# Performance work log

Hardware: AMD Instinct MI355X
Metric: run time of the kernel (lower is better)

## Reference

```python
import jax, jax.numpy as jnp
import numpy as np

B, NU, NT = 128, 32, 64          # batch, users/sample, antennas/sample
IN_F, H, OUT_F, NL = 128, 128, 16, 2
N_U, N_A = B * NU, B * NT        # total user / antenna nodes


def setup_inputs() -> dict:
    key = jax.random.key(0)
    ks = iter(jax.random.split(key, 40))
    p = lambda shape: jax.random.normal(next(ks), shape, jnp.float32) * 0.05
    inp = {
        'user_feat': jax.random.normal(next(ks), (N_U, IN_F), jnp.float32),
        'ant_noise': jax.random.normal(next(ks), (N_A, H), jnp.float32),
    }
    # complete bipartite edges within each batch sample
    b = np.arange(B)[:, None, None]
    u = np.arange(NU)[None, :, None]
    t = np.arange(NT)[None, None, :]
    su = np.broadcast_to(b * NU + u, (B, NU, NT)).reshape(-1)  # user global ids
    dt = np.broadcast_to(b * NT + t, (B, NU, NT)).reshape(-1)  # antenna global ids
    inp['src_u2a'] = jnp.asarray(su, jnp.int32)
    inp['dst_u2a'] = jnp.asarray(dt, jnp.int32)
    inp['src_a2u'] = jnp.asarray(dt, jnp.int32)
    inp['dst_a2u'] = jnp.asarray(su, jnp.int32)
    inp['W_ue'] = p((IN_F, H)); inp['b_ue'] = p((H,))
    inp['W_t'] = p((H, H));     inp['b_t'] = p((H,))
    for name in ['ca_aggr', 'ca_self', 'ca_comb', 'cu_aggr', 'cu_self', 'cu_comb']:
        inp[name + '_W'] = p((NL, H, H))
        inp[name + '_b'] = p((NL, H))
    inp['W_norm'] = p((H, OUT_F)); inp['b_norm'] = p((OUT_F,))
    return inp


def mlp(x, W, b):
    # stack of NL Linear(H,H) + ReLU, as in MLP module
    for i in range(W.shape[0]):
        x = jax.nn.relu(x @ W[i] + b[i])
    return x


def rel_conv(src_f, dst_f, src_idx, dst_idx, n_dst, aW, ab, sW, sb, cW, cb):
    # GraphConv2: mean-aggregate mlp_aggr(src) over in-edges, combine with mlp_self(dst)
    msg = mlp(src_f, aW, ab)                                   # [n_src, H]
    summed = jax.ops.segment_sum(msg[src_idx], dst_idx, num_segments=n_dst)
    deg = jax.ops.segment_sum(jnp.ones(dst_idx.shape, jnp.float32), dst_idx,
                              num_segments=n_dst)
    mean = summed / jnp.maximum(deg, 1.0)[:, None]
    return mlp(mlp(dst_f, sW, sb) + mean, cW, cb)


def reference(user_feat, ant_noise, src_u2a, dst_u2a, src_a2u, dst_a2u,
              W_ue, b_ue, W_t, b_t,
              ca_aggr_W, ca_aggr_b, ca_self_W, ca_self_b, ca_comb_W, ca_comb_b,
              cu_aggr_W, cu_aggr_b, cu_self_W, cu_self_b, cu_comb_W, cu_comb_b,
              W_norm, b_norm):
    # InitLayer
    hu = jax.nn.relu(user_feat @ W_ue + b_ue)                  # [B*NU, H]
    ant = jax.nn.relu(hu.reshape(B, NU, H).mean(axis=1) @ W_t + b_t)  # [B, H]
    ha = jnp.repeat(ant, NT, axis=0) + ant_noise               # [B*NT, H]
    # two applications of the SAME HeteroGraphConv (shared weights)
    for _ in range(2):
        na = rel_conv(hu, ha, src_u2a, dst_u2a, N_A,
                      ca_aggr_W, ca_aggr_b, ca_self_W, ca_self_b, ca_comb_W, ca_comb_b)
        nu = rel_conv(ha, hu, src_a2u, dst_a2u, N_U,
                      cu_aggr_W, cu_aggr_b, cu_self_W, cu_self_b, cu_comb_W, cu_comb_b)
        hu, ha = nu, na
    # NormLayer: project, split real/imag, normalize to unit modulus
    y = (ha @ W_norm + b_norm).reshape(B, NT, OUT_F)
    rf = OUT_F // 2
    re, im = y[..., :rf], y[..., rf:]
    mag = jnp.sqrt(re * re + im * im)
    return jnp.concatenate([re / mag, im / mag], axis=-1)      # [B, NT, OUT_F]
```

## Files before the change

kernel.cpp:

```cpp
#include <hip/hip_runtime.h>
#include <math.h>


using frag  = __attribute__((ext_vector_type(8))) short;
using f32x4 = __attribute__((ext_vector_type(4))) float;

#define LDST 136
#define SCOPE_AGT __HIP_MEMORY_SCOPE_AGENT

__device__ __forceinline__ float  bf2f(ushort u) { return __uint_as_float(((unsigned)u) << 16); }
__device__ __forceinline__ ushort f2bf(float f) {
    unsigned u = __float_as_uint(f);
    u += 0x7fff + ((u >> 16) & 1);
    return (ushort)(u >> 16);
}
__device__ __forceinline__ void gst4_sc(void* p, unsigned v) {
    asm volatile("global_store_dword %0, %1, off sc1" :: "v"(p), "v"(v) : "memory");
}

struct GP {
    const float *uf, *noise, *b_ue, *W_t, *b_t;
    const float *bias6[6];
    const float *Wn, *bn;
    const ushort *Wp;
    float *out;
    float *pE, *pA0, *pU0, *pA1;
    unsigned *flg;
};

struct PrepP { const float* Wm[13]; ushort* Wp; };

__global__ __launch_bounds__(512) void k_prep(PrepP Q)
{
    const int t  = blockIdx.x * 512 + threadIdx.x;
    const int j  = t & 7, l = (t >> 3) & 63, w = (t >> 9) & 7,
              kc = (t >> 12) & 3, m = t >> 14;
    const float v = Q.Wm[m][(kc * 32 + (l >> 4) * 8 + j) * 128 + w * 16 + (l & 15)];
    Q.Wp[t] = f2bf(v);
}

__device__ __forceinline__ void psync(unsigned* myf, unsigned* pf, unsigned s) {
    asm volatile("s_waitcnt vmcnt(0)" ::: "memory");
    __syncthreads();
    if (threadIdx.x == 0) {
        __hip_atomic_store(myf, s, __ATOMIC_RELAXED, SCOPE_AGT);
        while (__hip_atomic_load(pf, __ATOMIC_RELAXED, SCOPE_AGT) < s)
            __builtin_amdgcn_s_sleep(1);
    }
    __syncthreads();
}

struct AF { frag f[4]; };
__device__ __forceinline__ AF ldA(const ushort* __restrict__ Wp, int mat, int tid)
{
    AF a;
    const ushort* base = Wp + ((size_t)mat << 14) + (tid << 3);
#pragma unroll
    for (int kc = 0; kc < 4; ++kc)
        a.f[kc] = *(const frag*)(base + (kc << 12));
    return a;
}

template<int MT, bool MEANADD>
__device__ __forceinline__ void mlp_stage(const AF& A, const ushort* Xl, ushort* Yl,
    const float* biasL, const float* meanL, int n0, int l15, int q)
{
    const float4 bv = *(const float4*)(biasL + n0 + q * 4);
    float4 mv = {0.f, 0.f, 0.f, 0.f};
    if (MEANADD) mv = *(const float4*)(meanL + n0 + q * 4);
#pragma unroll
    for (int mt = 0; mt < MT; ++mt) {
        frag Bv[4];
#pragma unroll
        for (int kc = 0; kc < 4; ++kc)
            Bv[kc] = *(const frag*)(Xl + (mt * 16 + l15) * LDST + kc * 32 + q * 8);
        f32x4 acc = {0.f, 0.f, 0.f, 0.f};
#pragma unroll
        for (int kc = 0; kc < 4; ++kc)
            acc = __builtin_amdgcn_mfma_f32_16x16x32_bf16(A.f[kc], Bv[kc], acc, 0, 0, 0);
        float v0 = acc[0] + bv.x, v1 = acc[1] + bv.y, v2 = acc[2] + bv.z, v3 = acc[3] + bv.w;
        v0 = v0 > 0.f ? v0 : 0.f; v1 = v1 > 0.f ? v1 : 0.f;
        v2 = v2 > 0.f ? v2 : 0.f; v3 = v3 > 0.f ? v3 : 0.f;
        if (MEANADD) { v0 += mv.x; v1 += mv.y; v2 += mv.z; v3 += mv.w; }
        ushort4 o = { f2bf(v0), f2bf(v1), f2bf(v2), f2bf(v3) };
        *(ushort4*)(Yl + (mt * 16 + l15) * LDST + n0 + q * 4) = o;
    }
}

template<int ROWS>
__device__ __forceinline__ void colsum(const ushort* buf, float* redL,
                                       float* ownDst, float* __restrict__ gDst)
{
    const int t = threadIdx.x, g = t >> 7, col = t & 127;
    float s = 0.f;
#pragma unroll
    for (int r = g; r < ROWS; r += 4) s += bf2f(buf[r * LDST + col]);
    redL[g * 128 + col] = s;
    __syncthreads();
    if (t < 128) {
        float tot = redL[t] + redL[128 + t] + redL[256 + t] + redL[384 + t];
        ownDst[t] = tot;
        gst4_sc(gDst + t, __float_as_uint(tot));
    }
    __syncthreads();
}

__global__ __launch_bounds__(512, 1) void k_gnn(GP P)
{
    __shared__ __align__(16) ushort HU[16 * LDST];
    __shared__ __align__(16) ushort HA[32 * LDST];
    __shared__ __align__(16) ushort T0[32 * LDST];
    __shared__ __align__(16) ushort T1[32 * LDST];
    __shared__ __align__(16) float  biasL[1792];
    __shared__ __align__(16) float  redL[512];
    __shared__ __align__(16) float  meanP[128], meanQ[128], antL[128];

    const int blk = blockIdx.x, tid = threadIdx.x;
    const int b = blk & 127, half = blk >> 7, prt = blk ^ 128;
    const int lane = tid & 63, wave = tid >> 6;
    const int q = lane >> 4, l15 = lane & 15;
    const int n0 = wave * 16;
    unsigned* myf = P.flg + blk * 32;
    unsigned* prf = P.flg + prt * 32;

    AF An = ldA(P.Wp, 12, tid);

    {
        const int r = tid >> 5, k4 = tid & 31;
        const float4 v = *(const float4*)(P.uf + (size_t)(b * 32 + half * 16 + r) * 128 + k4 * 4);
        ushort4 o = { f2bf(v.x), f2bf(v.y), f2bf(v.z), f2bf(v.w) };
        *(ushort4*)(T0 + r * LDST + k4 * 4) = o;
    }
#pragma unroll
    for (int c = tid; c < 1024; c += 512) {
        const int r = c >> 5, k4 = c & 31;
        const float4 v = *(const float4*)(P.noise + (size_t)(b * 64 + half * 32 + r) * 128 + k4 * 4);
        ushort4 o = { f2bf(v.x), f2bf(v.y), f2bf(v.z), f2bf(v.w) };
        *(ushort4*)(HA + r * LDST + k4 * 4) = o;
    }
    if (tid < 128) biasL[tid] = P.b_ue[tid];
    if (tid < 128) biasL[1664 + tid] = P.b_t[tid];
#pragma unroll
    for (int r = 0; r < 6; ++r)
        if (tid < 256) biasL[128 + r * 256 + tid] = P.bias6[r][tid];
    __syncthreads();

    AF A;
    A = An; An = ldA(P.Wp, 0, tid);
    mlp_stage<1, false>(A, T0, HU, biasL + 0, nullptr, n0, l15, q);
    __syncthreads();
    colsum<16>(HU, redL, meanP, P.pE + blk * 128);
    A = An; An = ldA(P.Wp, 1, tid);
    mlp_stage<1, false>(A, HU, T0, biasL + 128, nullptr, n0, l15, q);
    __syncthreads();
    A = An; An = ldA(P.Wp, 6, tid);
    mlp_stage<1, false>(A, T0, T1, biasL + 256, nullptr, n0, l15, q);
    __syncthreads();
    colsum<16>(T1, redL, meanQ, P.pA0 + blk * 128);
    psync(myf, prf, 1u);

    if (tid < 128) {
        meanP[tid] = (meanP[tid] + P.pE[prt * 128 + tid]) * (1.f / 32.f);
        meanQ[tid] = (meanQ[tid] + P.pA0[prt * 128 + tid]) * (1.f / 32.f);
    }
    __syncthreads();
    {
        const int g = tid >> 7, col = tid & 127;
        float s = 0.f;
#pragma unroll 4
        for (int k = g * 32; k < g * 32 + 32; ++k) s += meanP[k] * P.W_t[k * 128 + col];
        redL[g * 128 + col] = s;
    }
    __syncthreads();
    if (tid < 128) {
        float a = biasL[1664 + tid] + redL[tid] + redL[128 + tid] + redL[256 + tid] + redL[384 + tid];
        antL[tid] = a > 0.f ? a : 0.f;
    }
    __syncthreads();
#pragma unroll
    for (int c = tid; c < 1024; c += 512) {
        const int r = c >> 5, k4 = c & 31;
        ushort4 h = *(ushort4*)(HA + r * LDST + k4 * 4);
        ushort4 o = { f2bf(bf2f(h.x) + antL[k4 * 4 + 0]), f2bf(bf2f(h.y) + antL[k4 * 4 + 1]),
                      f2bf(bf2f(h.z) + antL[k4 * 4 + 2]), f2bf(bf2f(h.w) + antL[k4 * 4 + 3]) };
        *(ushort4*)(HA + r * LDST + k4 * 4) = o;
    }
    __syncthreads();

    A = An; An = ldA(P.Wp, 7, tid);
    mlp_stage<2, false>(A, HA, T0, biasL + 896, nullptr, n0, l15, q);
    __syncthreads();
    A = An; An = ldA(P.Wp, 2, tid);
    mlp_stage<2, false>(A, T0, T1, biasL + 1024, nullptr, n0, l15, q);
    __syncthreads();
    colsum<32>(T1, redL, meanP, P.pU0 + blk * 128);
    A = An; An = ldA(P.Wp, 3, tid);
    mlp_stage<2, false>(A, HA, T0, biasL + 384, nullptr, n0, l15, q);
    __syncthreads();
    psync(myf, prf, 2u);
    if (tid < 128)
        meanP[tid] = (meanP[tid] + P.pU0[prt * 128 + tid]) * (1.f / 64.f);
    __syncthreads();
    A = An; An = ldA(P.Wp, 4, tid);
    mlp_stage<2, true >(A, T0, T1, biasL + 512, meanQ, n0, l15, q);
    __syncthreads();
    A = An; An = ldA(P.Wp, 5, tid);
    mlp_stage<2, false>(A, T1, T0, biasL + 640, nullptr, n0, l15, q);
    __syncthreads();
    A = An; An = ldA(P.Wp, 8, tid);
    mlp_stage<2, false>(A, T0, HA, biasL + 768, nullptr, n0, l15, q);
    __syncthreads();
    A = An; An = ldA(P.Wp, 9, tid);
    mlp_stage<1, false>(A, HU, T0, biasL + 1152, nullptr, n0, l15, q);
    __syncthreads();
    A = An; An = ldA(P.Wp, 10, tid);
    mlp_stage<1, true >(A, T0, T1, biasL + 1280, meanP, n0, l15, q);
    __syncthreads();
    A = An; An = ldA(P.Wp, 11, tid);
    mlp_stage<1, false>(A, T1, T0, biasL + 1408, nullptr, n0, l15, q);
    __syncthreads();
    A = An; An = ldA(P.Wp, 0, tid);
    mlp_stage<1, false>(A, T0, HU, biasL + 1536, nullptr, n0, l15, q);
    __syncthreads();

    A = An; An = ldA(P.Wp, 1, tid);
    mlp_stage<1, false>(A, HU, T0, biasL + 128, nullptr, n0, l15, q);
    __syncthreads();
    A = An; An = ldA(P.Wp, 2, tid);
    mlp_stage<1, false>(A, T0, T1, biasL + 256, nullptr, n0, l15, q);
    __syncthreads();
    colsum<16>(T1, redL, meanQ, P.pA1 + blk * 128);
    A = An; An = ldA(P.Wp, 3, tid);
    mlp_stage<2, false>(A, HA, T0, biasL + 384, nullptr, n0, l15, q);
    __syncthreads();
    psync(myf, prf, 3u);
    if (tid < 128)
        meanQ[tid] = (meanQ[tid] + P.pA1[prt * 128 + tid]) * (1.f / 32.f);
    __syncthreads();
    A = An; An = ldA(P.Wp, 4, tid);
    mlp_stage<2, true >(A, T0, T1, biasL + 512, meanQ, n0, l15, q);
    __syncthreads();
    A = An; An = ldA(P.Wp, 5, tid);
    mlp_stage<2, false>(A, T1, T0, biasL + 640, nullptr, n0, l15, q);
    __syncthreads();
    A = An;
    mlp_stage<2, false>(A, T0, T1, biasL + 768, nullptr, n0, l15, q);
    __syncthreads();

    float* WnS = (float*)T0;
    *(float4*)(WnS + tid * 4) = *(const float4*)(P.Wn + tid * 4);
    __syncthreads();
    {
        const int row = tid >> 4, j = tid & 15;
        float acc = P.bn[j];
        const ushort* h = T1 + row * LDST;
#pragma unroll 8
        for (int k = 0; k < 128; ++k) acc += bf2f(h[k]) * WnS[k * 16 + j];
        const float other = __shfl_xor(acc, 8);
        const float mag = sqrtf(acc * acc + other * other);
        P.out[(size_t)(b * 64 + half * 32 + row) * 16 + j] = acc / mag;
    }
}

extern "C" void kernel_launch(void* const* d_in, const int* in_sizes, int n_in,
                              void* d_out, int out_size, void* d_ws, size_t ws_size,
                              hipStream_t stream)
{
    GP P;
    P.uf    = (const float*)d_in[0];
    P.noise = (const float*)d_in[1];
    const float* W_ue = (const float*)d_in[6];
    P.b_ue  = (const float*)d_in[7];
    P.W_t   = (const float*)d_in[8];
    P.b_t   = (const float*)d_in[9];
    const float* caW[3] = {(const float*)d_in[10], (const float*)d_in[12], (const float*)d_in[14]};
    const float* cab[3] = {(const float*)d_in[11], (const float*)d_in[13], (const float*)d_in[15]};
    const float* cuW[3] = {(const float*)d_in[16], (const float*)d_in[18], (const float*)d_in[20]};
    const float* cub[3] = {(const float*)d_in[17], (const float*)d_in[19], (const float*)d_in[21]};
    P.Wn  = (const float*)d_in[22];
    P.bn  = (const float*)d_in[23];
    P.out = (float*)d_out;

    PrepP Q;
    Q.Wm[0]  = caW[0]; Q.Wm[1]  = caW[0] + 16384;
    Q.Wm[2]  = caW[1]; Q.Wm[3]  = caW[1] + 16384;
    Q.Wm[4]  = caW[2]; Q.Wm[5]  = caW[2] + 16384;
    Q.Wm[6]  = cuW[0]; Q.Wm[7]  = cuW[0] + 16384;
    Q.Wm[8]  = cuW[1]; Q.Wm[9]  = cuW[1] + 16384;
    Q.Wm[10] = cuW[2]; Q.Wm[11] = cuW[2] + 16384;
    Q.Wm[12] = W_ue;
    P.bias6[0] = cab[0]; P.bias6[1] = cab[1]; P.bias6[2] = cab[2];
    P.bias6[3] = cub[0]; P.bias6[4] = cub[1]; P.bias6[5] = cub[2];

    char* w = (char*)d_ws;
    P.flg = (unsigned*)w;
    P.pE  = (float*)(w + 32768);
    P.pA0 = P.pE  + 256 * 128;
    P.pU0 = P.pA0 + 256 * 128;
    P.pA1 = P.pU0 + 256 * 128;
    ushort* Wp = (ushort*)(w + 32768 + 4 * 256 * 128 * 4);
    Q.Wp = Wp;
    P.Wp = Wp;

    k_prep<<<dim3(416), dim3(512), 0, stream>>>(Q);
    hipMemsetAsync(w, 0, 32768, stream);
    k_gnn<<<dim3(256), dim3(512), 0, stream>>>(P);
}
```

Baseline: 124.8 us.

## Fuse column sums into MLP epilogue, pack bf16 conversions, fold flag reset into prep

Column sums are now computed from fp32 accumulators inside the MLP stage epilogue with wave shuffles, so the separate LDS column-sum pass and its two barriers go away. Float-to-bf16 conversion uses the hardware packed v_cvt_pk_bf16_f32 instruction instead of manual rounding. The weight prep kernel now handles eight elements per thread with 16-byte stores (fewer blocks) and also zeroes the sync flags, which removes the separate memset launch. Column sums are now taken before bf16 rounding, so the means differ slightly from the old ones.

```diff
diff --git a/kernel.cpp b/kernel.cpp
--- a/kernel.cpp
+++ b/kernel.cpp
@@ -14,8 +14,13 @@
     u += 0x7fff + ((u >> 16) & 1);
     return (ushort)(u >> 16);
 }
-__device__ __forceinline__ void gst4_sc(void* p, unsigned v) {
-    asm volatile("global_store_dword %0, %1, off sc1" :: "v"(p), "v"(v) : "memory");
+__device__ __forceinline__ unsigned cvtpk(float lo, float hi) {
+    unsigned r;
+    asm("v_cvt_pk_bf16_f32 %0, %1, %2" : "=v"(r) : "v"(lo), "v"(hi));
+    return r;
+}
+__device__ __forceinline__ void gst16_sc(void* p, f32x4 v) {
+    asm volatile("global_store_dwordx4 %0, %1, off sc1" :: "v"(p), "v"(v) : "memory");
 }
 
 struct GP {
@@ -28,15 +33,21 @@
     unsigned *flg;
 };
 
-struct PrepP { const float* Wm[13]; ushort* Wp; };
+struct PrepP { const float* Wm[13]; ushort* Wp; unsigned* flg; };
 
 __global__ __launch_bounds__(512) void k_prep(PrepP Q)
 {
-    const int t  = blockIdx.x * 512 + threadIdx.x;
-    const int j  = t & 7, l = (t >> 3) & 63, w = (t >> 9) & 7,
-              kc = (t >> 12) & 3, m = t >> 14;
-    const float v = Q.Wm[m][(kc * 32 + (l >> 4) * 8 + j) * 128 + w * 16 + (l & 15)];
-    Q.Wp[t] = f2bf(v);
+    const int tid = threadIdx.x, blk = blockIdx.x;
+    if (blk < 16) Q.flg[blk * 512 + tid] = 0;
+    const int e = (blk * 512 + tid) * 8;
+    const int l = (e >> 3) & 63, w = (e >> 9) & 7, kc = (e >> 12) & 3, m = e >> 14;
+    const float* src = Q.Wm[m] + (kc * 32 + (l >> 4) * 8) * 128 + w * 16 + (l & 15);
+    ushort h[8];
+#pragma unroll
+    for (int j = 0; j < 8; ++j) h[j] = f2bf(src[j * 128]);
+    uint4 o = { (unsigned)h[0] | ((unsigned)h[1] << 16), (unsigned)h[2] | ((unsigned)h[3] << 16),
+                (unsigned)h[4] | ((unsigned)h[5] << 16), (unsigned)h[6] | ((unsigned)h[7] << 16) };
+    *(uint4*)(Q.Wp + e) = o;
 }
 
 __device__ __forceinline__ void psync(unsigned* myf, unsigned* pf, unsigned s) {
@@ -61,13 +72,15 @@
     return a;
 }
 
-template<int MT, bool MEANADD>
+template<int MT, bool MEANADD, bool CS>
 __device__ __forceinline__ void mlp_stage(const AF& A, const ushort* Xl, ushort* Yl,
-    const float* biasL, const float* meanL, int n0, int l15, int q)
+    const float* biasL, const float* meanL, float* csL, float* __restrict__ csG,
+    int n0, int l15, int q)
 {
     const float4 bv = *(const float4*)(biasL + n0 + q * 4);
     float4 mv = {0.f, 0.f, 0.f, 0.f};
     if (MEANADD) mv = *(const float4*)(meanL + n0 + q * 4);
+    float cs0 = 0.f, cs1 = 0.f, cs2 = 0.f, cs3 = 0.f;
 #pragma unroll
     for (int mt = 0; mt < MT; ++mt) {
         frag Bv[4];
@@ -82,27 +95,22 @@
         v0 = v0 > 0.f ? v0 : 0.f; v1 = v1 > 0.f ? v1 : 0.f;
         v2 = v2 > 0.f ? v2 : 0.f; v3 = v3 > 0.f ? v3 : 0.f;
         if (MEANADD) { v0 += mv.x; v1 += mv.y; v2 += mv.z; v3 += mv.w; }
-        ushort4 o = { f2bf(v0), f2bf(v1), f2bf(v2), f2bf(v3) };
-        *(ushort4*)(Yl + (mt * 16 + l15) * LDST + n0 + q * 4) = o;
-    }
-}
-
-template<int ROWS>
-__device__ __forceinline__ void colsum(const ushort* buf, float* redL,
-                                       float* ownDst, float* __restrict__ gDst)
-{
-    const int t = threadIdx.x, g = t >> 7, col = t & 127;
-    float s = 0.f;
-#pragma unroll
-    for (int r = g; r < ROWS; r += 4) s += bf2f(buf[r * LDST + col]);
-    redL[g * 128 + col] = s;
-    __syncthreads();
-    if (t < 128) {
-        float tot = redL[t] + redL[128 + t] + redL[256 + t] + redL[384 + t];
-        ownDst[t] = tot;
-        gst4_sc(gDst + t, __float_as_uint(tot));
-    }
-    __syncthreads();
+        if (CS) { cs0 += v0; cs1 += v1; cs2 += v2; cs3 += v3; }
+        uint2 o = { cvtpk(v0, v1), cvtpk(v2, v3) };
+        *(uint2*)(Yl + (mt * 16 + l15) * LDST + n0 + q * 4) = o;
+    }
+    if (CS) {
+#pragma unroll
+        for (int m = 1; m <= 8; m <<= 1) {
+            cs0 += __shfl_xor(cs0, m); cs1 += __shfl_xor(cs1, m);
+            cs2 += __shfl_xor(cs2, m); cs3 += __shfl_xor(cs3, m);
+        }
+        if (l15 == 0) {
+            f32x4 t = { cs0, cs1, cs2, cs3 };
+            *(f32x4*)(csL + n0 + q * 4) = t;
+            gst16_sc(csG + n0 + q * 4, t);
+        }
+    }
 }
 
 __global__ __launch_bounds__(512, 1) void k_gnn(GP P)
@@ -128,15 +136,15 @@
     {
         const int r = tid >> 5, k4 = tid & 31;
         const float4 v = *(const float4*)(P.uf + (size_t)(b * 32 + half * 16 + r) * 128 + k4 * 4);
-        ushort4 o = { f2bf(v.x), f2bf(v.y), f2bf(v.z), f2bf(v.w) };
-        *(ushort4*)(T0 + r * LDST + k4 * 4) = o;
+        uint2 o = { cvtpk(v.x, v.y), cvtpk(v.z, v.w) };
+        *(uint2*)(T0 + r * LDST + k4 * 4) = o;
     }
 #pragma unroll
     for (int c = tid; c < 1024; c += 512) {
         const int r = c >> 5, k4 = c & 31;
         const float4 v = *(const float4*)(P.noise + (size_t)(b * 64 + half * 32 + r) * 128 + k4 * 4);
-        ushort4 o = { f2bf(v.x), f2bf(v.y), f2bf(v.z), f2bf(v.w) };
-        *(ushort4*)(HA + r * LDST + k4 * 4) = o;
+        uint2 o = { cvtpk(v.x, v.y), cvtpk(v.z, v.w) };
+        *(uint2*)(HA + r * LDST + k4 * 4) = o;
     }
     if (tid < 128) biasL[tid] = P.b_ue[tid];
     if (tid < 128) biasL[1664 + tid] = P.b_t[tid];
@@ -147,16 +155,14 @@
 
     AF A;
     A = An; An = ldA(P.Wp, 0, tid);
-    mlp_stage<1, false>(A, T0, HU, biasL + 0, nullptr, n0, l15, q);
-    __syncthreads();
-    colsum<16>(HU, redL, meanP, P.pE + blk * 128);
+    mlp_stage<1, false, true>(A, T0, HU, biasL + 0, nullptr, meanP, P.pE + blk * 128, n0, l15, q);
+    __syncthreads();
     A = An; An = ldA(P.Wp, 1, tid);
-    mlp_stage<1, false>(A, HU, T0, biasL + 128, nullptr, n0, l15, q);
+    mlp_stage<1, false, false>(A, HU, T0, biasL + 128, nullptr, nullptr, nullptr, n0, l15, q);
     __syncthreads();
     A = An; An = ldA(P.Wp, 6, tid);
-    mlp_stage<1, false>(A, T0, T1, biasL + 256, nullptr, n0, l15, q);
-    __syncthreads();
-    colsum<16>(T1, redL, meanQ, P.pA0 + blk * 128);
+    mlp_stage<1, false, true>(A, T0, T1, biasL + 256, nullptr, meanQ, P.pA0 + blk * 128, n0, l15, q);
+    __syncthreads();
     psync(myf, prf, 1u);
 
     if (tid < 128) {
@@ -181,70 +187,68 @@
     for (int c = tid; c < 1024; c += 512) {
         const int r = c >> 5, k4 = c & 31;
         ushort4 h = *(ushort4*)(HA + r * LDST + k4 * 4);
-        ushort4 o = { f2bf(bf2f(h.x) + antL[k4 * 4 + 0]), f2bf(bf2f(h.y) + antL[k4 * 4 + 1]),
-                      f2bf(bf2f(h.z) + antL[k4 * 4 + 2]), f2bf(bf2f(h.w) + antL[k4 * 4 + 3]) };
-        *(ushort4*)(HA + r * LDST + k4 * 4) = o;
+        uint2 o = { cvtpk(bf2f(h.x) + antL[k4 * 4 + 0], bf2f(h.y) + antL[k4 * 4 + 1]),
+                    cvtpk(bf2f(h.z) + antL[k4 * 4 + 2], bf2f(h.w) + antL[k4 * 4 + 3]) };
+        *(uint2*)(HA + r * LDST + k4 * 4) = o;
     }
     __syncthreads();
 
     A = An; An = ldA(P.Wp, 7, tid);
-    mlp_stage<2, false>(A, HA, T0, biasL + 896, nullptr, n0, l15, q);
+    mlp_stage<2, false, false>(A, HA, T0, biasL + 896, nullptr, nullptr, nullptr, n0, l15, q);
     __syncthreads();
     A = An; An = ldA(P.Wp, 2, tid);
-    mlp_stage<2, false>(A, T0, T1, biasL + 1024, nullptr, n0, l15, q);
-    __syncthreads();
-    colsum<32>(T1, redL, meanP, P.pU0 + blk * 128);
+    mlp_stage<2, false, true>(A, T0, T1, biasL + 1024, nullptr, meanP, P.pU0 + blk * 128, n0, l15, q);
+    __syncthreads();
     A = An; An = ldA(P.Wp, 3, tid);
-    mlp_stage<2, false>(A, HA, T0, biasL + 384, nullptr, n0, l15, q);
+    mlp_stage<2, false, false>(A, HA, T0, biasL + 384, nullptr, nullptr, nullptr, n0, l15, q);
     __syncthreads();
     psync(myf, prf, 2u);
     if (tid < 128)
         meanP[tid] = (meanP[tid] + P.pU0[prt * 128 + tid]) * (1.f / 64.f);
     __syncthreads();
     A = An; An = ldA(P.Wp, 4, tid);
-    mlp_stage<2, true >(A, T0, T1, biasL + 512, meanQ, n0, l15, q);
+    mlp_stage<2, true , false>(A, T0, T1, biasL + 512, meanQ, nullptr, nullptr, n0, l15, q);
     __syncthreads();
     A = An; An = ldA(P.Wp, 5, tid);
-    mlp_stage<2, false>(A, T1, T0, biasL + 640, nullptr, n0, l15, q);
+    mlp_stage<2, false, false>(A, T1, T0, biasL + 640, nullptr, nullptr, nullptr, n0, l15, q);
     __syncthreads();
     A = An; An = ldA(P.Wp, 8, tid);
-    mlp_stage<2, false>(A, T0, HA, biasL + 768, nullptr, n0, l15, q);
+    mlp_stage<2, false, false>(A, T0, HA, biasL + 768, nullptr, nullptr, nullptr, n0, l15, q);
     __syncthreads();
     A = An; An = ldA(P.Wp, 9, tid);
-    mlp_stage<1, false>(A, HU, T0, biasL + 1152, nullptr, n0, l15, q);
+    mlp_stage<1, false, false>(A, HU, T0, biasL + 1152, nullptr, nullptr, nullptr, n0, l15, q);
     __syncthreads();
     A = An; An = ldA(P.Wp, 10, tid);
-    mlp_stage<1, true >(A, T0, T1, biasL + 1280, meanP, n0, l15, q);
+    mlp_stage<1, true , false>(A, T0, T1, biasL + 1280, meanP, nullptr, nullptr, n0, l15, q);
     __syncthreads();
     A = An; An = ldA(P.Wp, 11, tid);
-    mlp_stage<1, false>(A, T1, T0, biasL + 1408, nullptr, n0, l15, q);
+    mlp_stage<1, false, false>(A, T1, T0, biasL + 1408, nullptr, nullptr, nullptr, n0, l15, q);
     __syncthreads();
     A = An; An = ldA(P.Wp, 0, tid);
-    mlp_stage<1, false>(A, T0, HU, biasL + 1536, nullptr, n0, l15, q);
+    mlp_stage<1, false, false>(A, T0, HU, biasL + 1536, nullptr, nullptr, nullptr, n0, l15, q);
     __syncthreads();
 
     A = An; An = ldA(P.Wp, 1, tid);
-    mlp_stage<1, false>(A, HU, T0, biasL + 128, nullptr, n0, l15, q);
+    mlp_stage<1, false, false>(A, HU, T0, biasL + 128, nullptr, nullptr, nullptr, n0, l15, q);
     __syncthreads();
     A = An; An = ldA(P.Wp, 2, tid);
-    mlp_stage<1, false>(A, T0, T1, biasL + 256, nullptr, n0, l15, q);
-    __syncthreads();
-    colsum<16>(T1, redL, meanQ, P.pA1 + blk * 128);
+    mlp_stage<1, false, true>(A, T0, T1, biasL + 256, nullptr, meanQ, P.pA1 + blk * 128, n0, l15, q);
+    __syncthreads();
     A = An; An = ldA(P.Wp, 3, tid);
-    mlp_stage<2, false>(A, HA, T0, biasL + 384, nullptr, n0, l15, q);
+    mlp_stage<2, false, false>(A, HA, T0, biasL + 384, nullptr, nullptr, nullptr, n0, l15, q);
     __syncthreads();
     psync(myf, prf, 3u);
     if (tid < 128)
         meanQ[tid] = (meanQ[tid] + P.pA1[prt * 128 + tid]) * (1.f / 32.f);
     __syncthreads();
     A = An; An = ldA(P.Wp, 4, tid);
-    mlp_stage<2, true >(A, T0, T1, biasL + 512, meanQ, n0, l15, q);
+    mlp_stage<2, true , false>(A, T0, T1, biasL + 512, meanQ, nullptr, nullptr, n0, l15, q);
     __syncthreads();
     A = An; An = ldA(P.Wp, 5, tid);
-    mlp_stage<2, false>(A, T1, T0, biasL + 640, nullptr, n0, l15, q);
+    mlp_stage<2, false, false>(A, T1, T0, biasL + 640, nullptr, nullptr, nullptr, n0, l15, q);
     __syncthreads();
     A = An;
-    mlp_stage<2, false>(A, T0, T1, biasL + 768, nullptr, n0, l15, q);
+    mlp_stage<2, false, false>(A, T0, T1, biasL + 768, nullptr, nullptr, nullptr, n0, l15, q);
     __syncthreads();
 
     float* WnS = (float*)T0;
@@ -300,9 +304,9 @@
     P.pA1 = P.pU0 + 256 * 128;
     ushort* Wp = (ushort*)(w + 32768 + 4 * 256 * 128 * 4);
     Q.Wp = Wp;
+    Q.flg = P.flg;
     P.Wp = Wp;
 
-    k_prep<<<dim3(416), dim3(512), 0, stream>>>(Q);
-    hipMemsetAsync(w, 0, 32768, stream);
+    k_prep<<<dim3(52), dim3(512), 0, stream>>>(Q);
     k_gnn<<<dim3(256), dim3(512), 0, stream>>>(P);
 }
```

Result: faster. 121.9 us (-2.3%).
